# Kernel optimization log

Measured on AMD Instinct MI355X. Metric: run time of the kernel, lower is better.

## Reference

```python
import jax, jax.numpy as jnp
import numpy as np

# Constants matching init_kwargs
N_HEADS = 8
D_MODEL = 256
PATCH_NUM = 128
D_K = D_MODEL // N_HEADS  # 32
TEMP = 0.5
EPS = 1e-10


def setup_inputs() -> dict:
    key = jax.random.key(0)
    ks = jax.random.split(key, 20)
    s = 0.02
    d, h, n = D_MODEL, N_HEADS, PATCH_NUM
    inp = {
        "x": jax.random.normal(ks[0], (32, n, d), dtype=jnp.float32),
        "gumbel_u": jax.random.uniform(ks[1], (h, n, n, 2), dtype=jnp.float32),
        "memory_w": jax.random.normal(ks[2], (n, h * d), dtype=jnp.float32) * s,
        "fc_out_w": jax.random.normal(ks[3], (2 * d, d), dtype=jnp.float32) * s,
        "fc_out_b": jnp.zeros((d,), jnp.float32),
        "fc_cat_w": jax.random.normal(ks[4], (d, 2), dtype=jnp.float32) * s,
        "fc_cat_b": jnp.zeros((2,), jnp.float32),
        "wq": jax.random.normal(ks[5], (d, d), dtype=jnp.float32) * s,
        "bq": jnp.zeros((d,), jnp.float32),
        "wk": jax.random.normal(ks[6], (d, d), dtype=jnp.float32) * s,
        "bk": jnp.zeros((d,), jnp.float32),
        "wv": jax.random.normal(ks[7], (d, d), dtype=jnp.float32) * s,
        "bv": jnp.zeros((d,), jnp.float32),
        "out_w": jax.random.normal(ks[8], (d, d), dtype=jnp.float32) * s,
        "out_b": jnp.zeros((d,), jnp.float32),
        "mlp_w1": jax.random.normal(ks[9], (d, d), dtype=jnp.float32) * s,
        "mlp_b1": jnp.zeros((d,), jnp.float32),
        "mlp_w2": jax.random.normal(ks[10], (d, d), dtype=jnp.float32) * s,
        "mlp_b2": jnp.zeros((d,), jnp.float32),
    }
    return inp


def _forward(x, memory_w, fc_out_w, fc_out_b, fc_cat_w, fc_cat_b,
             wq, bq, wk, bk, wv, bv, out_w, out_b,
             mlp_w1, mlp_b1, mlp_w2, mlp_b2, gumbel_u):
    H, N, D = N_HEADS, PATCH_NUM, D_MODEL
    B = x.shape[0]

    # ---- SSConnectionLearning on memory feats ----
    # memory: Embedding(N, d_model*n_heads) -> feats [H, N, D]
    feats = memory_w.reshape(N, H, D).transpose(1, 0, 2)
    # rel_rec gathers row index i (receiver), rel_send gathers col index j (sender)
    senders = jnp.broadcast_to(feats[:, None, :, :], (H, N, N, D))   # feats[j]
    receivers = jnp.broadcast_to(feats[:, :, None, :], (H, N, N, D))  # feats[i]
    pair = jnp.concatenate([senders, receivers], axis=-1)  # [H,N,N,2D]
    hdn = jax.nn.relu(jnp.einsum('hijc,cd->hijd', pair, fc_out_w) + fc_out_b)
    logits = jnp.einsum('hijd,dk->hijk', hdn, fc_cat_w) + fc_cat_b  # [H,N,N,2]

    # gumbel-softmax, hard=True, straight-through
    g = -jnp.log(-jnp.log(gumbel_u + EPS) + EPS)
    y_soft = jax.nn.softmax((logits + g) / TEMP, axis=-1)
    y_hard = jax.nn.one_hot(jnp.argmax(y_soft, axis=-1), 2, dtype=y_soft.dtype)
    y = jax.lax.stop_gradient(y_hard - y_soft) + y_soft
    conn = y[..., 1]  # [H,N,N] learned sparse connection mask

    # ---- PatchIntegration (GELU MLP, dropout = identity in eval) ----
    xm = jax.nn.gelu(x @ mlp_w1 + mlp_b1)
    xm = xm @ mlp_w2 + mlp_b2

    # ---- Multihead attention masked by connection matrix ----
    q = (xm @ wq + bq).reshape(B, N, H, D_K).transpose(0, 2, 1, 3)  # [B,H,N,dk]
    k = (xm @ wk + bk).reshape(B, N, H, D_K).transpose(0, 2, 1, 3)
    v = (xm @ wv + bv).reshape(B, N, H, D_K).transpose(0, 2, 1, 3)
    scale = D_K ** -0.5
    scores = jnp.einsum('bhqd,bhkd->bhqk', q, k) * scale
    # additive mask: blocked where conn==0 (large negative keeps softmax finite)
    scores = scores + (conn[None] - 1.0) * 1e9
    attn = jax.nn.softmax(scores, axis=-1)
    out = jnp.einsum('bhqk,bhkd->bhqd', attn, v)
    out = out.transpose(0, 2, 1, 3).reshape(B, N, H * D_K)
    out = out @ out_w + out_b
    return out


def reference(x, gumbel_u, memory_w, fc_out_w, fc_out_b, fc_cat_w, fc_cat_b,
              wq, bq, wk, bk, wv, bv, out_w, out_b,
              mlp_w1, mlp_b1, mlp_w2, mlp_b2):
    return _forward(x, memory_w, fc_out_w, fc_out_b, fc_cat_w, fc_cat_b,
                    wq, bq, wk, bk, wv, bv, out_w, out_b,
                    mlp_w1, mlp_b1, mlp_w2, mlp_b2, gumbel_u)
```

## Files before the change

### kernel.cpp

```cpp
#include <hip/hip_runtime.h>
#include <hip/hip_bf16.h>
#include <math.h>


typedef short short8 __attribute__((ext_vector_type(8)));
typedef float f32x4 __attribute__((ext_vector_type(4)));

union V8 { uint4 u; short8 s; };

__device__ __forceinline__ float gelu_f(float x) {
    float inner = 0.7978845608028654f * (x + 0.044715f * x * x * x);
    return 0.5f * x * (1.0f + tanhf(inner));
}
__device__ __forceinline__ void split_bf16(float x, ushort& h, ushort& l) {
    __hip_bfloat16 bh = __float2bfloat16(x);
    float hf = __bfloat162float(bh);
    __hip_bfloat16 bl = __float2bfloat16(x - hf);
    h = __builtin_bit_cast(ushort, bh);
    l = __builtin_bit_cast(ushort, bl);
}
__device__ __forceinline__ ushort bf16bits(float x) {
    return __builtin_bit_cast(ushort, __float2bfloat16(x));
}
__device__ __forceinline__ float bits_to_f(ushort v) {
    return __builtin_bit_cast(float, ((uint)v) << 16);
}
__device__ __forceinline__ short8 lds_frag(const ushort* p) {
    V8 v; v.u = *(const uint4*)p; return v.s;
}


__global__ __launch_bounds__(512) void k_wprep(
    const float* __restrict__ mlp_w1, const float* __restrict__ mlp_w2,
    const float* __restrict__ wq, const float* __restrict__ wk,
    const float* __restrict__ wv, const float* __restrict__ out_w,
    const float* __restrict__ fc_out_w,
    ushort* __restrict__ hi, ushort* __restrict__ lo) {
    __shared__ __align__(16) float xs[32 * 132];
    int bx = blockIdx.x, t = threadIdx.x;
    int m = bx >> 4, ks = (bx >> 1) & 7, nh = bx & 1;
    const float* W = m == 0 ? mlp_w1 : m == 1 ? mlp_w2 : m == 2 ? wq :
                     m == 3 ? wk : m == 4 ? wv : m == 5 ? out_w :
                     m == 6 ? fc_out_w : fc_out_w + 65536;
    ushort* Hm = hi + m * 65536;
    ushort* Lm = lo + m * 65536;
    #pragma unroll
    for (int p = 0; p < 2; ++p) {
        int idx = p * 512 + t;
        int row = idx >> 5, c4 = (idx & 31) * 4;
        *(float4*)(xs + row * 132 + c4) =
            *(const float4*)(W + (ks * 32 + row) * 256 + nh * 128 + c4);
    }
    __syncthreads();
    int lane = t & 63, w = t >> 6, lr = lane & 15, quad = lane >> 4;
    int tg = nh * 8 + w;
    int nl = w * 16 + lr;
    ushort hb[8], lb[8];
    #pragma unroll
    for (int j = 0; j < 8; ++j)
        split_bf16(xs[(quad * 8 + j) * 132 + nl], hb[j], lb[j]);
    uint4 ph = { (uint)hb[0] | ((uint)hb[1] << 16), (uint)hb[2] | ((uint)hb[3] << 16),
                 (uint)hb[4] | ((uint)hb[5] << 16), (uint)hb[6] | ((uint)hb[7] << 16) };
    uint4 pl = { (uint)lb[0] | ((uint)lb[1] << 16), (uint)lb[2] | ((uint)lb[3] << 16),
                 (uint)lb[4] | ((uint)lb[5] << 16), (uint)lb[6] | ((uint)lb[7] << 16) };
    int idx = ((tg * 8 + ks) * 64 + lane) * 8;
    *(uint4*)(Hm + idx) = ph;
    *(uint4*)(Lm + idx) = pl;
}

__global__ __launch_bounds__(512) void k_p2(
    const float* __restrict__ memory_w, const float* __restrict__ X,
    const ushort* __restrict__ Whi, const ushort* __restrict__ Wlo,
    const float* __restrict__ b1, const float* __restrict__ b2,
    const float* __restrict__ Bq, const float* __restrict__ Bk,
    const float* __restrict__ Bv,
    float* __restrict__ A, float* __restrict__ Bm,
    ushort* __restrict__ Qn, ushort* __restrict__ Kn, ushort* __restrict__ Vt) {
    __shared__ __align__(16) struct {
        ushort aHi[16 * 264], aLo[16 * 264];
        ushort bHi[16 * 264], bLo[16 * 264];
    } sm;
    int bx = blockIdx.x, t = threadIdx.x;
    int lane = t & 63, w = t >> 6, lr = lane & 15, quad = lane >> 4;

    {
        int rt = bx >> 2;
        #pragma unroll
        for (int ii = 0; ii < 2; ++ii) {
            int f4 = ii * 512 + t;
            int rr = f4 >> 6, c = (f4 & 63) * 4;
            int r = rt * 16 + rr;
            int hh = r >> 7, n = r & 127;
            float4 xv = *(const float4*)(memory_w + n * 2048 + hh * 256 + c);
            ushort h4[4], l4[4];
            split_bf16(xv.x, h4[0], l4[0]); split_bf16(xv.y, h4[1], l4[1]);
            split_bf16(xv.z, h4[2], l4[2]); split_bf16(xv.w, h4[3], l4[3]);
            uint2 ph = { (uint)h4[0] | ((uint)h4[1] << 16), (uint)h4[2] | ((uint)h4[3] << 16) };
            uint2 pl = { (uint)l4[0] | ((uint)l4[1] << 16), (uint)l4[2] | ((uint)l4[3] << 16) };
            *(uint2*)(sm.aHi + rr * 264 + c) = ph;
            *(uint2*)(sm.aLo + rr * 264 + c) = pl;
        }
        __syncthreads();
        int task = (bx & 3) * 8 + w;
        int msel = task >> 4, tg = task & 15;
        const uint4* H4 = (const uint4*)(Whi + (6 + msel) * 65536);
        const uint4* L4 = (const uint4*)(Wlo + (6 + msel) * 65536);
        const ushort* ah = sm.aHi + lr * 264 + quad * 8;
        const ushort* al = sm.aLo + lr * 264 + quad * 8;
        float* O = msel ? Bm : A;
        f32x4 acc = {};
        #pragma unroll
        for (int ks = 0; ks < 8; ++ks) {
            short8 a_h = lds_frag(ah + ks * 32);
            short8 a_l = lds_frag(al + ks * 32);
            int off = (tg * 8 + ks) * 64 + lane;
            V8 bh, bl; bh.u = H4[off]; bl.u = L4[off];
            acc = __builtin_amdgcn_mfma_f32_16x16x32_bf16(a_h, bh.s, acc, 0, 0, 0);
            acc = __builtin_amdgcn_mfma_f32_16x16x32_bf16(a_l, bh.s, acc, 0, 0, 0);
            acc = __builtin_amdgcn_mfma_f32_16x16x32_bf16(a_h, bl.s, acc, 0, 0, 0);
        }
        int n0 = tg * 16 + lr;
        #pragma unroll
        for (int r = 0; r < 4; ++r)
            O[(rt * 16 + quad * 4 + r) * 256 + n0] = acc[r];
        __syncthreads();
    }

    int r0 = bx * 16;
    #pragma unroll
    for (int ii = 0; ii < 2; ++ii) {
        int f4 = ii * 512 + t;
        int row = f4 >> 6, c = (f4 & 63) * 4;
        float4 xv = *(const float4*)(X + (r0 + row) * 256 + c);
        ushort h4[4], l4[4];
        split_bf16(xv.x, h4[0], l4[0]); split_bf16(xv.y, h4[1], l4[1]);
        split_bf16(xv.z, h4[2], l4[2]); split_bf16(xv.w, h4[3], l4[3]);
        uint2 ph = { (uint)h4[0] | ((uint)h4[1] << 16), (uint)h4[2] | ((uint)h4[3] << 16) };
        uint2 pl = { (uint)l4[0] | ((uint)l4[1] << 16), (uint)l4[2] | ((uint)l4[3] << 16) };
        *(uint2*)(sm.aHi + row * 264 + c) = ph;
        *(uint2*)(sm.aLo + row * 264 + c) = pl;
    }
    __syncthreads();
    int aoff = lr * 264 + quad * 8;
    {
        const uint4* H4 = (const uint4*)(Whi + 0 * 65536);
        const uint4* L4 = (const uint4*)(Wlo + 0 * 65536);
        f32x4 acc[2] = {};
        #pragma unroll
        for (int ks = 0; ks < 8; ++ks) {
            short8 a_h = lds_frag(sm.aHi + aoff + ks * 32);
            short8 a_l = lds_frag(sm.aLo + aoff + ks * 32);
            #pragma unroll
            for (int ti = 0; ti < 2; ++ti) {
                int off = ((w * 2 + ti) * 8 + ks) * 64 + lane;
                V8 bh, bl; bh.u = H4[off]; bl.u = L4[off];
                acc[ti] = __builtin_amdgcn_mfma_f32_16x16x32_bf16(a_h, bh.s, acc[ti], 0, 0, 0);
                acc[ti] = __builtin_amdgcn_mfma_f32_16x16x32_bf16(a_l, bh.s, acc[ti], 0, 0, 0);
                acc[ti] = __builtin_amdgcn_mfma_f32_16x16x32_bf16(a_h, bl.s, acc[ti], 0, 0, 0);
            }
        }
        #pragma unroll
        for (int ti = 0; ti < 2; ++ti) {
            int n0 = (w * 2 + ti) * 16 + lr;
            float bb = b1[n0];
            #pragma unroll
            for (int r = 0; r < 4; ++r) {
                float o = gelu_f(acc[ti][r] + bb);
                ushort hh, ll; split_bf16(o, hh, ll);
                int ad = (quad * 4 + r) * 264 + n0;
                sm.bHi[ad] = hh; sm.bLo[ad] = ll;
            }
        }
    }
    __syncthreads();
    {
        const uint4* H4 = (const uint4*)(Whi + 1 * 65536);
        const uint4* L4 = (const uint4*)(Wlo + 1 * 65536);
        f32x4 acc[2] = {};
        #pragma unroll
        for (int ks = 0; ks < 8; ++ks) {
            short8 a_h = lds_frag(sm.bHi + aoff + ks * 32);
            short8 a_l = lds_frag(sm.bLo + aoff + ks * 32);
            #pragma unroll
            for (int ti = 0; ti < 2; ++ti) {
                int off = ((w * 2 + ti) * 8 + ks) * 64 + lane;
                V8 bh, bl; bh.u = H4[off]; bl.u = L4[off];
                acc[ti] = __builtin_amdgcn_mfma_f32_16x16x32_bf16(a_h, bh.s, acc[ti], 0, 0, 0);
                acc[ti] = __builtin_amdgcn_mfma_f32_16x16x32_bf16(a_l, bh.s, acc[ti], 0, 0, 0);
                acc[ti] = __builtin_amdgcn_mfma_f32_16x16x32_bf16(a_h, bl.s, acc[ti], 0, 0, 0);
            }
        }
        __syncthreads();
        #pragma unroll
        for (int ti = 0; ti < 2; ++ti) {
            int n0 = (w * 2 + ti) * 16 + lr;
            float bb = b2[n0];
            #pragma unroll
            for (int r = 0; r < 4; ++r) {
                float o = acc[ti][r] + bb;
                ushort hh, ll; split_bf16(o, hh, ll);
                int ad = (quad * 4 + r) * 264 + n0;
                sm.aHi[ad] = hh; sm.aLo[ad] = ll;
            }
        }
    }
    __syncthreads();
    {
        const uint4* Hq = (const uint4*)(Whi + 2 * 65536);
        const uint4* Lq = (const uint4*)(Wlo + 2 * 65536);
        const uint4* Hk = (const uint4*)(Whi + 3 * 65536);
        const uint4* Lk = (const uint4*)(Wlo + 3 * 65536);
        const uint4* Hv = (const uint4*)(Whi + 4 * 65536);
        const uint4* Lv = (const uint4*)(Wlo + 4 * 65536);
        f32x4 aq[2] = {}, ak[2] = {}, av[2] = {};
        #pragma unroll 2
        for (int ks = 0; ks < 8; ++ks) {
            short8 a_h = lds_frag(sm.aHi + aoff + ks * 32);
            short8 a_l = lds_frag(sm.aLo + aoff + ks * 32);
            #pragma unroll
            for (int ti = 0; ti < 2; ++ti) {
                int off = ((w * 2 + ti) * 8 + ks) * 64 + lane;
                V8 qh, ql, kh, kl, vh, vl;
                qh.u = Hq[off]; ql.u = Lq[off];
                kh.u = Hk[off]; kl.u = Lk[off];
                vh.u = Hv[off]; vl.u = Lv[off];
                aq[ti] = __builtin_amdgcn_mfma_f32_16x16x32_bf16(a_h, qh.s, aq[ti], 0, 0, 0);
                aq[ti] = __builtin_amdgcn_mfma_f32_16x16x32_bf16(a_l, qh.s, aq[ti], 0, 0, 0);
                aq[ti] = __builtin_amdgcn_mfma_f32_16x16x32_bf16(a_h, ql.s, aq[ti], 0, 0, 0);
                ak[ti] = __builtin_amdgcn_mfma_f32_16x16x32_bf16(a_h, kh.s, ak[ti], 0, 0, 0);
                ak[ti] = __builtin_amdgcn_mfma_f32_16x16x32_bf16(a_l, kh.s, ak[ti], 0, 0, 0);
                ak[ti] = __builtin_amdgcn_mfma_f32_16x16x32_bf16(a_h, kl.s, ak[ti], 0, 0, 0);
                av[ti] = __builtin_amdgcn_mfma_f32_16x16x32_bf16(a_h, vh.s, av[ti], 0, 0, 0);
                av[ti] = __builtin_amdgcn_mfma_f32_16x16x32_bf16(a_l, vh.s, av[ti], 0, 0, 0);
                av[ti] = __builtin_amdgcn_mfma_f32_16x16x32_bf16(a_h, vl.s, av[ti], 0, 0, 0);
            }
        }
        #pragma unroll
        for (int ti = 0; ti < 2; ++ti) {
            int n0 = (w * 2 + ti) * 16 + lr;
            int hh = n0 >> 5, dk = n0 & 31;
            float vbq = Bq[n0], vbk = Bk[n0], vbv = Bv[n0];
            #pragma unroll
            for (int r = 0; r < 4; ++r) {
                int row = r0 + quad * 4 + r;
                int bb = row >> 7, n = row & 127;
                int bh_ = bb * 8 + hh;
                Qn[(bh_ * 128 + n) * 32 + dk] = bf16bits(aq[ti][r] + vbq);
                Kn[(bh_ * 128 + n) * 32 + dk] = bf16bits(ak[ti][r] + vbk);
                Vt[(bh_ * 32 + dk) * 128 + n] = bf16bits(av[ti][r] + vbv);
            }
        }
    }
}

__global__ __launch_bounds__(512) void k_conn(
    const float* __restrict__ A, const float* __restrict__ Bmat,
    const float* __restrict__ fc_out_b, const float* __restrict__ fc_cat_w,
    const float* __restrict__ fc_cat_b, const float* __restrict__ gumbel_u,
    ushort* __restrict__ maskb) {
    __shared__ __align__(16) float sA[16 * 260], sB[32 * 260];
    int bx = blockIdx.x, t = threadIdx.x;
    int h = bx >> 5;
    int rem = bx & 31;
    int it = rem >> 3, jt = rem & 7;
    int i0 = it * 32, j0 = jt * 16;
    int jl = t & 15, il = t >> 4;
    #pragma unroll
    for (int p = 0; p < 6; ++p) {
        int id2 = p * 512 + t;
        if (id2 < 1024) {
            int rr = id2 >> 6, c = (id2 & 63) * 4;
            *(float4*)(sA + rr * 260 + c) =
                *(const float4*)(A + (h * 128 + j0 + rr) * 256 + c);
        } else {
            int id3 = id2 - 1024;
            int rr = id3 >> 6, c = (id3 & 63) * 4;
            float4 bv = *(const float4*)(Bmat + (h * 128 + i0 + rr) * 256 + c);
            float4 fb = *(const float4*)(fc_out_b + c);
            bv.x += fb.x; bv.y += fb.y; bv.z += fb.z; bv.w += fb.w;
            *(float4*)(sB + rr * 260 + c) = bv;
        }
    }
    __syncthreads();
    const float* Ar = sA + jl * 260;
    const float* Br = sB + il * 260;
    float l0 = fc_cat_b[0], l1 = fc_cat_b[1];
    #pragma unroll 4
    for (int d4 = 0; d4 < 64; ++d4) {
        int d = d4 * 4;
        float4 av = *(const float4*)(Ar + d);
        float4 bv = *(const float4*)(Br + d);
        float4 cwA = *(const float4*)(fc_cat_w + d * 2);
        float4 cwB = *(const float4*)(fc_cat_w + d * 2 + 4);
        float h0 = fmaxf(av.x + bv.x, 0.f);
        float h1 = fmaxf(av.y + bv.y, 0.f);
        float h2 = fmaxf(av.z + bv.z, 0.f);
        float h3 = fmaxf(av.w + bv.w, 0.f);
        l0 += h0 * cwA.x + h1 * cwA.z + h2 * cwB.x + h3 * cwB.z;
        l1 += h0 * cwA.y + h1 * cwA.w + h2 * cwB.y + h3 * cwB.w;
    }
    int i = i0 + il, j = j0 + jl;
    float2 uu = *(const float2*)(gumbel_u + ((h * 128 + i) * 128 + j) * 2);
    float g0 = -logf(-logf(uu.x + 1e-10f) + 1e-10f);
    float g1 = -logf(-logf(uu.y + 1e-10f) + 1e-10f);
    bool on = (l1 + g1) > (l0 + g0);
    maskb[(h * 128 + i) * 128 + j] = bf16bits(on ? 0.f : -1e9f);
}

__global__ __launch_bounds__(512) void k_attn_mfma(
    const ushort* __restrict__ Qn, const ushort* __restrict__ Kn,
    const ushort* __restrict__ Vt, const ushort* __restrict__ maskb,
    ushort* __restrict__ aoHi, ushort* __restrict__ aoLo) {
    __shared__ __align__(16) ushort ps[2][64 * 136];
    int bx = blockIdx.x, t = threadIdx.x;
    int lane = t & 63, w = t >> 6, lr = lane & 15, quad = lane >> 4;
    int jh = t >> 8;
    int job = bx * 2 + jh;
    int b = job >> 4, h = (job >> 1) & 7, rh = job & 1;
    int w4 = w & 3;
    int rt = rh * 4 + w4;
    int bh_ = b * 8 + h;
    ushort* psj = ps[jh];
    V8 af;
    af.u = *(const uint4*)(Qn + (bh_ * 128 + rt * 16 + lr) * 32 + quad * 8);
    f32x4 s[8];
    #pragma unroll
    for (int ct = 0; ct < 8; ++ct) {
        V8 bf_;
        bf_.u = *(const uint4*)(Kn + (bh_ * 128 + ct * 16 + lr) * 32 + quad * 8);
        f32x4 z = {0.f, 0.f, 0.f, 0.f};
        s[ct] = __builtin_amdgcn_mfma_f32_16x16x32_bf16(af.s, bf_.s, z, 0, 0, 0);
    }
    const float scale = 0.17677669529663687f;
    const ushort* mrow = maskb + h * 16384;
    #pragma unroll
    for (int r = 0; r < 4; ++r) {
        int lrow = w4 * 16 + quad * 4 + r;
        int grow = rt * 16 + quad * 4 + r;
        float sv[8];
        float mx = -3.0e38f;
        #pragma unroll
        for (int ct = 0; ct < 8; ++ct) {
            float bias = bits_to_f(mrow[grow * 128 + ct * 16 + lr]);
            sv[ct] = s[ct][r] * scale + bias;
            mx = fmaxf(mx, sv[ct]);
        }
        mx = fmaxf(mx, __shfl_xor(mx, 1));
        mx = fmaxf(mx, __shfl_xor(mx, 2));
        mx = fmaxf(mx, __shfl_xor(mx, 4));
        mx = fmaxf(mx, __shfl_xor(mx, 8));
        float sum = 0.f;
        #pragma unroll
        for (int ct = 0; ct < 8; ++ct) {
            sv[ct] = __expf(sv[ct] - mx);
            sum += sv[ct];
        }
        sum += __shfl_xor(sum, 1);
        sum += __shfl_xor(sum, 2);
        sum += __shfl_xor(sum, 4);
        sum += __shfl_xor(sum, 8);
        float iv = 1.f / sum;
        #pragma unroll
        for (int ct = 0; ct < 8; ++ct)
            psj[lrow * 136 + ct * 16 + lr] = bf16bits(sv[ct] * iv);
    }
    f32x4 o0 = {}, o1 = {};
    #pragma unroll
    for (int kk = 0; kk < 4; ++kk) {
        short8 pa = lds_frag(psj + (w4 * 16 + lr) * 136 + kk * 32 + quad * 8);
        V8 v0, v1;
        v0.u = *(const uint4*)(Vt + (bh_ * 32 + lr) * 128 + kk * 32 + quad * 8);
        v1.u = *(const uint4*)(Vt + (bh_ * 32 + 16 + lr) * 128 + kk * 32 + quad * 8);
        o0 = __builtin_amdgcn_mfma_f32_16x16x32_bf16(pa, v0.s, o0, 0, 0, 0);
        o1 = __builtin_amdgcn_mfma_f32_16x16x32_bf16(pa, v1.s, o1, 0, 0, 0);
    }
    #pragma unroll
    for (int r = 0; r < 4; ++r) {
        int grow = rt * 16 + quad * 4 + r;
        int base = (b * 128 + grow) * 256 + h * 32;
        ushort hh, ll;
        split_bf16(o0[r], hh, ll);
        aoHi[base + lr] = hh; aoLo[base + lr] = ll;
        split_bf16(o1[r], hh, ll);
        aoHi[base + 16 + lr] = hh; aoLo[base + 16 + lr] = ll;
    }
}

__global__ __launch_bounds__(512) void k_gemm16(
    const ushort* __restrict__ aoHi, const ushort* __restrict__ aoLo,
    const ushort* __restrict__ Whi, const ushort* __restrict__ Wlo,
    const float* __restrict__ bias, float* __restrict__ Y) {
    int t = threadIdx.x;
    int lane = t & 63, w = t >> 6, lr = lane & 15, quad = lane >> 4;
    int r0 = blockIdx.x * 16;
    const uint4* H4 = (const uint4*)Whi;
    const uint4* L4 = (const uint4*)Wlo;
    f32x4 acc[2] = {};
    #pragma unroll
    for (int ks = 0; ks < 8; ++ks) {
        V8 ahv, alv;
        ahv.u = *(const uint4*)(aoHi + (r0 + lr) * 256 + ks * 32 + quad * 8);
        alv.u = *(const uint4*)(aoLo + (r0 + lr) * 256 + ks * 32 + quad * 8);
        #pragma unroll
        for (int ti = 0; ti < 2; ++ti) {
            int off = ((w * 2 + ti) * 8 + ks) * 64 + lane;
            V8 bh, bl; bh.u = H4[off]; bl.u = L4[off];
            acc[ti] = __builtin_amdgcn_mfma_f32_16x16x32_bf16(ahv.s, bh.s, acc[ti], 0, 0, 0);
            acc[ti] = __builtin_amdgcn_mfma_f32_16x16x32_bf16(alv.s, bh.s, acc[ti], 0, 0, 0);
            acc[ti] = __builtin_amdgcn_mfma_f32_16x16x32_bf16(ahv.s, bl.s, acc[ti], 0, 0, 0);
        }
    }
    #pragma unroll
    for (int ti = 0; ti < 2; ++ti) {
        int n0 = (w * 2 + ti) * 16 + lr;
        float bs = bias[n0];
        #pragma unroll
        for (int r = 0; r < 4; ++r)
            Y[(r0 + quad * 4 + r) * 256 + n0] = acc[ti][r] + bs;
    }
}

extern "C" void kernel_launch(void* const* d_in, const int* in_sizes, int n_in,
                              void* d_out, int out_size, void* d_ws, size_t ws_size,
                              hipStream_t stream) {
    const float* x        = (const float*)d_in[0];
    const float* gumbel_u = (const float*)d_in[1];
    const float* memory_w = (const float*)d_in[2];
    const float* fc_out_w = (const float*)d_in[3];
    const float* fc_out_b = (const float*)d_in[4];
    const float* fc_cat_w = (const float*)d_in[5];
    const float* fc_cat_b = (const float*)d_in[6];
    const float* wq       = (const float*)d_in[7];
    const float* bq       = (const float*)d_in[8];
    const float* wk       = (const float*)d_in[9];
    const float* bk       = (const float*)d_in[10];
    const float* wv_      = (const float*)d_in[11];
    const float* bv_      = (const float*)d_in[12];
    const float* out_w    = (const float*)d_in[13];
    const float* out_b    = (const float*)d_in[14];
    const float* mlp_w1   = (const float*)d_in[15];
    const float* mlp_b1   = (const float*)d_in[16];
    const float* mlp_w2   = (const float*)d_in[17];
    const float* mlp_b2   = (const float*)d_in[18];

    float* ws     = (float*)d_ws;
    float* A      = ws;
    float* Bm     = ws + 262144;
    ushort* mask  = (ushort*)(ws + 524288);
    ushort* qn    = (ushort*)(ws + 589824);
    ushort* kn    = (ushort*)(ws + 1114112);
    ushort* vt    = (ushort*)(ws + 1638400);
    ushort* aoHi  = (ushort*)(ws + 2162688);
    ushort* aoLo  = (ushort*)(ws + 2686976);
    ushort* wf_hi = (ushort*)(ws + 3211264);
    ushort* wf_lo = wf_hi + 8 * 65536;
    float* out    = (float*)d_out;

    k_wprep<<<dim3(128), dim3(512), 0, stream>>>(
        mlp_w1, mlp_w2, wq, wk, wv_, out_w, fc_out_w, wf_hi, wf_lo);
    k_p2<<<dim3(256), dim3(512), 0, stream>>>(
        memory_w, x, wf_hi, wf_lo, mlp_b1, mlp_b2, bq, bk, bv_,
        A, Bm, qn, kn, vt);
    k_conn<<<dim3(256), dim3(512), 0, stream>>>(
        A, Bm, fc_out_b, fc_cat_w, fc_cat_b, gumbel_u, mask);
    k_attn_mfma<<<dim3(256), dim3(512), 0, stream>>>(qn, kn, vt, mask, aoHi, aoLo);
    k_gemm16<<<dim3(256), dim3(512), 0, stream>>>(aoHi, aoLo, wf_hi + 5 * 65536,
                                                  wf_lo + 5 * 65536, out_b, out);
}
```

Before: 154.9 us.

## Split memory-feature GEMM into dedicated blocks and halve weight-prep grid

k_p2 previously had every block do a slice of the memory-feature projection (A/Bm) before its x-MLP/QKV work. Now 64 extra blocks handle the memory GEMM alone, each computing 4 column tiles per wave, while the other 256 blocks do only the MLP/QKV path, with shared memory unioned between the two roles. k_wprep now packs two jobs per 512-thread block (256 threads each), so it launches 64 blocks instead of 128. This is meant to cut per-block serial latency and the extra barrier, at the cost of uneven block durations and a larger grid.

```diff
diff --git a/kernel.cpp b/kernel.cpp
--- a/kernel.cpp
+++ b/kernel.cpp
@@ -36,36 +36,43 @@
     const float* __restrict__ wv, const float* __restrict__ out_w,
     const float* __restrict__ fc_out_w,
     ushort* __restrict__ hi, ushort* __restrict__ lo) {
-    __shared__ __align__(16) float xs[32 * 132];
+    __shared__ __align__(16) float xs2[2][32 * 132];
     int bx = blockIdx.x, t = threadIdx.x;
-    int m = bx >> 4, ks = (bx >> 1) & 7, nh = bx & 1;
+    int half = t >> 8, tl = t & 255;
+    int job = bx * 2 + half;
+    int m = job >> 4, ks = (job >> 1) & 7, nh = job & 1;
     const float* W = m == 0 ? mlp_w1 : m == 1 ? mlp_w2 : m == 2 ? wq :
                      m == 3 ? wk : m == 4 ? wv : m == 5 ? out_w :
                      m == 6 ? fc_out_w : fc_out_w + 65536;
     ushort* Hm = hi + m * 65536;
     ushort* Lm = lo + m * 65536;
-    #pragma unroll
-    for (int p = 0; p < 2; ++p) {
-        int idx = p * 512 + t;
+    float* xs = xs2[half];
+    #pragma unroll
+    for (int p = 0; p < 4; ++p) {
+        int idx = p * 256 + tl;
         int row = idx >> 5, c4 = (idx & 31) * 4;
         *(float4*)(xs + row * 132 + c4) =
             *(const float4*)(W + (ks * 32 + row) * 256 + nh * 128 + c4);
     }
     __syncthreads();
-    int lane = t & 63, w = t >> 6, lr = lane & 15, quad = lane >> 4;
-    int tg = nh * 8 + w;
-    int nl = w * 16 + lr;
-    ushort hb[8], lb[8];
-    #pragma unroll
-    for (int j = 0; j < 8; ++j)
-        split_bf16(xs[(quad * 8 + j) * 132 + nl], hb[j], lb[j]);
-    uint4 ph = { (uint)hb[0] | ((uint)hb[1] << 16), (uint)hb[2] | ((uint)hb[3] << 16),
-                 (uint)hb[4] | ((uint)hb[5] << 16), (uint)hb[6] | ((uint)hb[7] << 16) };
-    uint4 pl = { (uint)lb[0] | ((uint)lb[1] << 16), (uint)lb[2] | ((uint)lb[3] << 16),
-                 (uint)lb[4] | ((uint)lb[5] << 16), (uint)lb[6] | ((uint)lb[7] << 16) };
-    int idx = ((tg * 8 + ks) * 64 + lane) * 8;
-    *(uint4*)(Hm + idx) = ph;
-    *(uint4*)(Lm + idx) = pl;
+    int lane = tl & 63, lr = lane & 15, quad = lane >> 4;
+    #pragma unroll
+    for (int it = 0; it < 2; ++it) {
+        int tgl = (tl >> 6) + 4 * it;
+        int tg = nh * 8 + tgl;
+        int nl = tgl * 16 + lr;
+        ushort hb[8], lb[8];
+        #pragma unroll
+        for (int j = 0; j < 8; ++j)
+            split_bf16(xs[(quad * 8 + j) * 132 + nl], hb[j], lb[j]);
+        uint4 ph = { (uint)hb[0] | ((uint)hb[1] << 16), (uint)hb[2] | ((uint)hb[3] << 16),
+                     (uint)hb[4] | ((uint)hb[5] << 16), (uint)hb[6] | ((uint)hb[7] << 16) };
+        uint4 pl = { (uint)lb[0] | ((uint)lb[1] << 16), (uint)lb[2] | ((uint)lb[3] << 16),
+                     (uint)lb[4] | ((uint)lb[5] << 16), (uint)lb[6] | ((uint)lb[7] << 16) };
+        int idx = ((tg * 8 + ks) * 64 + lane) * 8;
+        *(uint4*)(Hm + idx) = ph;
+        *(uint4*)(Lm + idx) = pl;
+    }
 }
 
 __global__ __launch_bounds__(512) void k_p2(
@@ -76,57 +83,63 @@
     const float* __restrict__ Bv,
     float* __restrict__ A, float* __restrict__ Bm,
     ushort* __restrict__ Qn, ushort* __restrict__ Kn, ushort* __restrict__ Vt) {
-    __shared__ __align__(16) struct {
-        ushort aHi[16 * 264], aLo[16 * 264];
-        ushort bHi[16 * 264], bLo[16 * 264];
+    __shared__ __align__(16) union {
+        struct { ushort xhi[16 * 264], xlo[16 * 264]; } f;
+        struct {
+            ushort aHi[16 * 264], aLo[16 * 264];
+            ushort bHi[16 * 264], bLo[16 * 264];
+        } g;
     } sm;
     int bx = blockIdx.x, t = threadIdx.x;
-    int lane = t & 63, w = t >> 6, lr = lane & 15, quad = lane >> 4;
-
-    {
-        int rt = bx >> 2;
+    if (bx < 64) {
+        int rt = bx;
         #pragma unroll
         for (int ii = 0; ii < 2; ++ii) {
             int f4 = ii * 512 + t;
             int rr = f4 >> 6, c = (f4 & 63) * 4;
             int r = rt * 16 + rr;
-            int hh = r >> 7, n = r & 127;
-            float4 xv = *(const float4*)(memory_w + n * 2048 + hh * 256 + c);
-            ushort h4[4], l4[4];
-            split_bf16(xv.x, h4[0], l4[0]); split_bf16(xv.y, h4[1], l4[1]);
-            split_bf16(xv.z, h4[2], l4[2]); split_bf16(xv.w, h4[3], l4[3]);
-            uint2 ph = { (uint)h4[0] | ((uint)h4[1] << 16), (uint)h4[2] | ((uint)h4[3] << 16) };
-            uint2 pl = { (uint)l4[0] | ((uint)l4[1] << 16), (uint)l4[2] | ((uint)l4[3] << 16) };
-            *(uint2*)(sm.aHi + rr * 264 + c) = ph;
-            *(uint2*)(sm.aLo + rr * 264 + c) = pl;
+            int h = r >> 7, n = r & 127;
+            float4 xv = *(const float4*)(memory_w + n * 2048 + h * 256 + c);
+            ushort hh[4], ll[4];
+            split_bf16(xv.x, hh[0], ll[0]); split_bf16(xv.y, hh[1], ll[1]);
+            split_bf16(xv.z, hh[2], ll[2]); split_bf16(xv.w, hh[3], ll[3]);
+            uint2 ph = { (uint)hh[0] | ((uint)hh[1] << 16), (uint)hh[2] | ((uint)hh[3] << 16) };
+            uint2 pl = { (uint)ll[0] | ((uint)ll[1] << 16), (uint)ll[2] | ((uint)ll[3] << 16) };
+            *(uint2*)(sm.f.xhi + rr * 264 + c) = ph;
+            *(uint2*)(sm.f.xlo + rr * 264 + c) = pl;
         }
         __syncthreads();
-        int task = (bx & 3) * 8 + w;
-        int msel = task >> 4, tg = task & 15;
+        int lane = t & 63, w = t >> 6;
+        int lr = lane & 15, quad = lane >> 4;
+        int msel = w & 1, cq = w >> 1;
         const uint4* H4 = (const uint4*)(Whi + (6 + msel) * 65536);
         const uint4* L4 = (const uint4*)(Wlo + (6 + msel) * 65536);
-        const ushort* ah = sm.aHi + lr * 264 + quad * 8;
-        const ushort* al = sm.aLo + lr * 264 + quad * 8;
+        const ushort* ah = sm.f.xhi + lr * 264 + quad * 8;
+        const ushort* al = sm.f.xlo + lr * 264 + quad * 8;
         float* O = msel ? Bm : A;
-        f32x4 acc = {};
-        #pragma unroll
-        for (int ks = 0; ks < 8; ++ks) {
-            short8 a_h = lds_frag(ah + ks * 32);
-            short8 a_l = lds_frag(al + ks * 32);
-            int off = (tg * 8 + ks) * 64 + lane;
-            V8 bh, bl; bh.u = H4[off]; bl.u = L4[off];
-            acc = __builtin_amdgcn_mfma_f32_16x16x32_bf16(a_h, bh.s, acc, 0, 0, 0);
-            acc = __builtin_amdgcn_mfma_f32_16x16x32_bf16(a_l, bh.s, acc, 0, 0, 0);
-            acc = __builtin_amdgcn_mfma_f32_16x16x32_bf16(a_h, bl.s, acc, 0, 0, 0);
-        }
-        int n0 = tg * 16 + lr;
-        #pragma unroll
-        for (int r = 0; r < 4; ++r)
-            O[(rt * 16 + quad * 4 + r) * 256 + n0] = acc[r];
-        __syncthreads();
-    }
-
-    int r0 = bx * 16;
+        #pragma unroll
+        for (int i = 0; i < 4; ++i) {
+            int tg = cq * 4 + i;
+            f32x4 acc = {};
+            #pragma unroll
+            for (int ks = 0; ks < 8; ++ks) {
+                short8 a_h = lds_frag(ah + ks * 32);
+                short8 a_l = lds_frag(al + ks * 32);
+                int off = (tg * 8 + ks) * 64 + lane;
+                V8 bh, bl; bh.u = H4[off]; bl.u = L4[off];
+                acc = __builtin_amdgcn_mfma_f32_16x16x32_bf16(a_h, bh.s, acc, 0, 0, 0);
+                acc = __builtin_amdgcn_mfma_f32_16x16x32_bf16(a_l, bh.s, acc, 0, 0, 0);
+                acc = __builtin_amdgcn_mfma_f32_16x16x32_bf16(a_h, bl.s, acc, 0, 0, 0);
+            }
+            int n0 = tg * 16 + lr;
+            #pragma unroll
+            for (int r = 0; r < 4; ++r)
+                O[(rt * 16 + quad * 4 + r) * 256 + n0] = acc[r];
+        }
+        return;
+    }
+    int r0 = (bx - 64) * 16;
+    int lane = t & 63, w = t >> 6, lr = lane & 15, quad = lane >> 4;
     #pragma unroll
     for (int ii = 0; ii < 2; ++ii) {
         int f4 = ii * 512 + t;
@@ -137,8 +150,8 @@
         split_bf16(xv.z, h4[2], l4[2]); split_bf16(xv.w, h4[3], l4[3]);
         uint2 ph = { (uint)h4[0] | ((uint)h4[1] << 16), (uint)h4[2] | ((uint)h4[3] << 16) };
         uint2 pl = { (uint)l4[0] | ((uint)l4[1] << 16), (uint)l4[2] | ((uint)l4[3] << 16) };
-        *(uint2*)(sm.aHi + row * 264 + c) = ph;
-        *(uint2*)(sm.aLo + row * 264 + c) = pl;
+        *(uint2*)(sm.g.aHi + row * 264 + c) = ph;
+        *(uint2*)(sm.g.aLo + row * 264 + c) = pl;
     }
     __syncthreads();
     int aoff = lr * 264 + quad * 8;
@@ -148,8 +161,8 @@
         f32x4 acc[2] = {};
         #pragma unroll
         for (int ks = 0; ks < 8; ++ks) {
-            short8 a_h = lds_frag(sm.aHi + aoff + ks * 32);
-            short8 a_l = lds_frag(sm.aLo + aoff + ks * 32);
+            short8 a_h = lds_frag(sm.g.aHi + aoff + ks * 32);
+            short8 a_l = lds_frag(sm.g.aLo + aoff + ks * 32);
             #pragma unroll
             for (int ti = 0; ti < 2; ++ti) {
                 int off = ((w * 2 + ti) * 8 + ks) * 64 + lane;
@@ -168,7 +181,7 @@
                 float o = gelu_f(acc[ti][r] + bb);
                 ushort hh, ll; split_bf16(o, hh, ll);
                 int ad = (quad * 4 + r) * 264 + n0;
-                sm.bHi[ad] = hh; sm.bLo[ad] = ll;
+                sm.g.bHi[ad] = hh; sm.g.bLo[ad] = ll;
             }
         }
     }
@@ -179,8 +192,8 @@
         f32x4 acc[2] = {};
         #pragma unroll
         for (int ks = 0; ks < 8; ++ks) {
-            short8 a_h = lds_frag(sm.bHi + aoff + ks * 32);
-            short8 a_l = lds_frag(sm.bLo + aoff + ks * 32);
+            short8 a_h = lds_frag(sm.g.bHi + aoff + ks * 32);
+            short8 a_l = lds_frag(sm.g.bLo + aoff + ks * 32);
             #pragma unroll
             for (int ti = 0; ti < 2; ++ti) {
                 int off = ((w * 2 + ti) * 8 + ks) * 64 + lane;
@@ -200,7 +213,7 @@
                 float o = acc[ti][r] + bb;
                 ushort hh, ll; split_bf16(o, hh, ll);
                 int ad = (quad * 4 + r) * 264 + n0;
-                sm.aHi[ad] = hh; sm.aLo[ad] = ll;
+                sm.g.aHi[ad] = hh; sm.g.aLo[ad] = ll;
             }
         }
     }
@@ -215,8 +228,8 @@
         f32x4 aq[2] = {}, ak[2] = {}, av[2] = {};
         #pragma unroll 2
         for (int ks = 0; ks < 8; ++ks) {
-            short8 a_h = lds_frag(sm.aHi + aoff + ks * 32);
-            short8 a_l = lds_frag(sm.aLo + aoff + ks * 32);
+            short8 a_h = lds_frag(sm.g.aHi + aoff + ks * 32);
+            short8 a_l = lds_frag(sm.g.aLo + aoff + ks * 32);
             #pragma unroll
             for (int ti = 0; ti < 2; ++ti) {
                 int off = ((w * 2 + ti) * 8 + ks) * 64 + lane;
@@ -456,9 +469,9 @@
     ushort* wf_lo = wf_hi + 8 * 65536;
     float* out    = (float*)d_out;
 
-    k_wprep<<<dim3(128), dim3(512), 0, stream>>>(
+    k_wprep<<<dim3(64), dim3(512), 0, stream>>>(
         mlp_w1, mlp_w2, wq, wk, wv_, out_w, fc_out_w, wf_hi, wf_lo);
-    k_p2<<<dim3(256), dim3(512), 0, stream>>>(
+    k_p2<<<dim3(320), dim3(512), 0, stream>>>(
         memory_w, x, wf_hi, wf_lo, mlp_b1, mlp_b2, bq, bk, bv_,
         A, Bm, qn, kn, vt);
     k_conn<<<dim3(256), dim3(512), 0, stream>>>(
```

Result: faster. 150.7 us (-2.7%).
